# Kernel tuning notes

Measured on AMD Instinct MI355X. Metric: run time of the kernel, lower is better.

Reference implementation:

```python
import jax, jax.numpy as jnp
import numpy as np

B, S, D_MODEL, D_K, D_V, N_HEAD = 2, 2048, 1024, 1024, 1024, 16


def setup_inputs() -> dict:
    key = jax.random.key(0)
    k1, k2, k3, k4, k5, k6, k7 = jax.random.split(key, 7)
    s = 1.0 / np.sqrt(D_MODEL)
    return {
        "q": jax.random.normal(k1, (B, S, D_MODEL), dtype=jnp.float32),
        "k": jax.random.normal(k2, (B, S, D_MODEL), dtype=jnp.float32),
        "v": jax.random.normal(k3, (B, S, D_MODEL), dtype=jnp.float32),
        "Wq": jax.random.normal(k4, (D_MODEL, D_K), dtype=jnp.float32) * s,
        "Wk": jax.random.normal(k5, (D_MODEL, D_K), dtype=jnp.float32) * s,
        "Wv": jax.random.normal(k6, (D_MODEL, D_V), dtype=jnp.float32) * s,
        "Wp": jax.random.normal(k7, (D_V, D_MODEL), dtype=jnp.float32) * (1.0 / np.sqrt(D_V)),
    }


def reference(q, k, v, Wq, Wk, Wv, Wp):
    b, sq, _ = q.shape
    sk = k.shape[1]
    hd_k = D_K // N_HEAD
    hd_v = D_V // N_HEAD
    # Faithful to original: plain row-major reshape (B,S,d) -> (B,H,S,d/H),
    # i.e. the sequence axis is split across heads (as torch .view does here).
    Q = (q @ Wq).reshape(b, N_HEAD, sq, hd_k)
    K = (k @ Wk).reshape(b, N_HEAD, sk, hd_k)
    V = (v @ Wv).reshape(b, N_HEAD, sk, hd_v)
    # No 1/sqrt(d_k) scaling in the original module.
    wei = jnp.einsum('bhqd,bhkd->bhqk', Q, K)
    # causal mask (masked=True): tril(ones(sq, sk))
    causal = jnp.arange(sq)[:, None] >= jnp.arange(sk)[None, :]
    wei = jnp.where(causal[None, None], wei, -jnp.inf)
    att = jnp.einsum('bhqk,bhkd->bhqd', jax.nn.softmax(wei, axis=-1), V)
    out = jnp.swapaxes(att, 1, 2).reshape(b, sq, D_V)
    return out @ Wp
```

## Files before the change

kernel.cpp:

```cpp
#include <hip/hip_runtime.h>
#include <cstdint>
#include <cstddef>


typedef _Float16 f16;
typedef _Float16 f16x8 __attribute__((ext_vector_type(8)));
typedef float f32x4 __attribute__((ext_vector_type(4)));

#define NB 2
#define NS 2048
#define NDM 1024
#define NHEAD 16

__device__ __forceinline__ void gload16(void* lds, const void* g) {
    __builtin_amdgcn_global_load_lds(
        (__attribute__((address_space(1))) void*)g,
        (__attribute__((address_space(3))) void*)lds, 16, 0, 0);
}

__device__ __forceinline__ float fast_exp2(float x) {
#if __has_builtin(__builtin_amdgcn_exp2f)
    return __builtin_amdgcn_exp2f(x);
#else
    return __expf(x * 0.69314718055994531f);
#endif
}

__global__ __launch_bounds__(256) void cast3_kernel(
    const float* __restrict__ s0, const float* __restrict__ s1, const float* __restrict__ s2,
    f16* __restrict__ d0, f16* __restrict__ d1, f16* __restrict__ d2, int nvec)
{
    const float* s = blockIdx.z == 0 ? s0 : (blockIdx.z == 1 ? s1 : s2);
    f16* d        = blockIdx.z == 0 ? d0 : (blockIdx.z == 1 ? d1 : d2);
    int vi = blockIdx.x * 256 + threadIdx.x;
    if (vi >= nvec) return;
    const float4* sp = (const float4*)s;
    float4 a = sp[vi * 2 + 0];
    float4 b = sp[vi * 2 + 1];
    f16x8 h;
    h[0] = (f16)a.x; h[1] = (f16)a.y; h[2] = (f16)a.z; h[3] = (f16)a.w;
    h[4] = (f16)b.x; h[5] = (f16)b.y; h[6] = (f16)b.z; h[7] = (f16)b.w;
    *(f16x8*)(d + (size_t)vi * 8) = h;
}

__global__ __launch_bounds__(256) void tcast4_kernel(
    const float* __restrict__ w0, const float* __restrict__ w1,
    const float* __restrict__ w2, const float* __restrict__ w3,
    f16* __restrict__ t0, f16* __restrict__ t1, f16* __restrict__ t2, f16* __restrict__ t3)
{
    const int n = 1024;
    const float* W; f16* T;
    switch (blockIdx.z) {
        case 0: W = w0; T = t0; break;
        case 1: W = w1; T = t1; break;
        case 2: W = w2; T = t2; break;
        default: W = w3; T = t3; break;
    }
    __shared__ float tile[32][33];
    int tx = threadIdx.x, ty = threadIdx.y;
    int c0 = blockIdx.x * 32, r0 = blockIdx.y * 32;
    #pragma unroll
    for (int i = 0; i < 32; i += 8)
        tile[ty + i][tx] = W[(size_t)(r0 + ty + i) * n + c0 + tx];
    __syncthreads();
    #pragma unroll
    for (int i = 0; i < 32; i += 8)
        T[(size_t)(c0 + ty + i) * n + r0 + tx] = (f16)tile[tx][ty + i];
}

template <typename CT>
__device__ __forceinline__ void gemm_abt_body(
    const f16* __restrict__ A, const f16* __restrict__ Bt, CT* __restrict__ C,
    int M, int N, int K, int bx, int by, float cscale)
{
    __shared__ f16 As[128][64];
    __shared__ f16 Bs[128][64];
    const int tid  = threadIdx.x;
    const int lane = tid & 63, wave = tid >> 6;
    const int quad = lane >> 4, ln = lane & 15;
    const int wm = wave >> 1, wn = wave & 1;
    const int m0 = by * 128, n0 = bx * 128;
    const int r8 = lane >> 3, c8 = lane & 7;
    const int swz = ((c8 ^ r8) * 8);

    f32x4 acc[4][4] = {};
    for (int k0 = 0; k0 < K; k0 += 64) {
        __syncthreads();
        #pragma unroll
        for (int i = 0; i < 4; i++) {
            int blk = wave * 4 + i;
            int row = blk * 8 + r8;
            gload16(&As[blk * 8][0], &A [(size_t)(m0 + row) * K + k0 + swz]);
            gload16(&Bs[blk * 8][0], &Bt[(size_t)(n0 + row) * K + k0 + swz]);
        }
        __syncthreads();
        #pragma unroll
        for (int kc = 0; kc < 2; kc++) {
            f16x8 af[4], bfr[4];
            #pragma unroll
            for (int mt = 0; mt < 4; mt++)
                af[mt] = *(const f16x8*)&As[wm * 64 + mt * 16 + ln][((kc * 4 + quad) ^ (ln & 7)) * 8];
            #pragma unroll
            for (int nt = 0; nt < 4; nt++)
                bfr[nt] = *(const f16x8*)&Bs[wn * 64 + nt * 16 + ln][((kc * 4 + quad) ^ (ln & 7)) * 8];
            #pragma unroll
            for (int mt = 0; mt < 4; mt++)
                #pragma unroll
                for (int nt = 0; nt < 4; nt++)
                    acc[mt][nt] = __builtin_amdgcn_mfma_f32_16x16x32_f16(af[mt], bfr[nt], acc[mt][nt], 0, 0, 0);
        }
    }
    #pragma unroll
    for (int mt = 0; mt < 4; mt++)
        #pragma unroll
        for (int nt = 0; nt < 4; nt++)
            #pragma unroll
            for (int r = 0; r < 4; r++) {
                int row = m0 + wm * 64 + mt * 16 + quad * 4 + r;
                int col = n0 + wn * 64 + nt * 16 + ln;
                C[(size_t)row * N + col] = (CT)(acc[mt][nt][r] * cscale);
            }
}

__global__ __launch_bounds__(256) void gemm3_kernel(
    const f16* __restrict__ a0, const f16* __restrict__ a1, const f16* __restrict__ a2,
    const f16* __restrict__ b0, const f16* __restrict__ b1, const f16* __restrict__ b2,
    f16* __restrict__ c0, f16* __restrict__ c1, f16* __restrict__ c2, int M, int N, int K)
{
    const f16 *A, *Bt; f16* C; float sc;
    switch (blockIdx.z) {
        case 0: A = a0; Bt = b0; C = c0; sc = 1.4426950408889634f; break;
        case 1: A = a1; Bt = b1; C = c1; sc = 1.0f; break;
        default: A = a2; Bt = b2; C = c2; sc = 1.0f; break;
    }
    gemm_abt_body<f16>(A, Bt, C, M, N, K, blockIdx.x, blockIdx.y, sc);
}

__global__ __launch_bounds__(256) void gemm_out_kernel(
    const f16* __restrict__ A, const f16* __restrict__ Bt, float* __restrict__ C, int M, int N, int K)
{
    gemm_abt_body<float>(A, Bt, C, M, N, K, blockIdx.x, blockIdx.y, 1.0f);
}

__global__ __launch_bounds__(256) void vtrans_kernel(
    const f16* __restrict__ Vp, f16* __restrict__ Vt)
{
    const int kt = blockIdx.x;
    const int h  = blockIdx.y;
    const int b  = blockIdx.z;
    const f16* src = Vp + (size_t)b * (NS * NDM) + (size_t)h * (128 * NDM);
    f16* dst = Vt + (size_t)(b * NHEAD + h) * (64 * 2048);

    __shared__ f16 Ls[64][64];
    const int tid = threadIdx.x;
    #pragma unroll
    for (int i = 0; i < 2; i++) {
        int vi = tid + i * 256;
        int key = vi >> 3, c = vi & 7;
        int cs = c ^ ((key >> 3) & 7);
        *(uint4*)&Ls[key][cs * 8] = *(const uint4*)&src[(size_t)(kt * 64 + key) * 64 + c * 8];
    }
    __syncthreads();
    #pragma unroll
    for (int i = 0; i < 2; i++) {
        int vi = tid + i * 256;
        int d2 = vi >> 3, kc = vi & 7;
        int cs = (d2 >> 3) ^ kc;
        f16 tmp[8];
        #pragma unroll
        for (int j = 0; j < 8; j++)
            tmp[j] = Ls[kc * 8 + j][cs * 8 + (d2 & 7)];
        *(uint4*)&dst[(size_t)d2 * 2048 + kt * 64 + kc * 8] = *(uint4*)tmp;
    }
}

__global__ __launch_bounds__(256) void attn_kernel(
    const f16* __restrict__ Qp, const f16* __restrict__ Kp, const f16* __restrict__ Vt,
    f16* __restrict__ att)
{
    const int p = blockIdx.x;
    const int h = blockIdx.y;
    const int b = blockIdx.z;
    const size_t hb = (size_t)b * (NS * NDM) + (size_t)h * (128 * NDM);
    const f16* Qh = Qp + hb;
    const f16* Kh = Kp + hb;
    const f16* Vh = Vt + (size_t)(b * NHEAD + h) * (64 * 2048);

    __shared__ f16 PQ[64][136];
    __shared__ f16 Ks[128][64];
    __shared__ f16 Vs[64][128];

    const int tid  = threadIdx.x;
    const int lane = tid & 63, wave = tid >> 6;
    const int quad = lane >> 4, ln = lane & 15;
    const int r8 = lane >> 3, c8 = lane & 7;
    const int r4 = lane >> 4, c16 = lane & 15;

    for (int pass = 0; pass < 2; pass++) {
        const int qt = pass == 0 ? (31 - p) : p;
        __syncthreads();
        #pragma unroll
        for (int i = 0; i < 2; i++) {
            int vi = tid + i * 256;
            int row = vi >> 3, kk = (vi & 7) * 8;
            *(uint4*)&PQ[row][kk] = *(const uint4*)&Qh[(size_t)(qt * 64 + row) * 64 + kk];
        }
        __syncthreads();
        f16x8 qf[2];
        #pragma unroll
        for (int kc = 0; kc < 2; kc++)
            qf[kc] = *(const f16x8*)&PQ[wave * 16 + ln][kc * 32 + quad * 8];

        float m_i[4], l_i[4];
        #pragma unroll
        for (int r = 0; r < 4; r++) { m_i[r] = -3e30f; l_i[r] = 0.f; }
        f32x4 o[4] = {};

        const int nkt = (qt + 2) >> 1;
        for (int kt = 0; kt < nkt; kt++) {
            __syncthreads();
            #pragma unroll
            for (int i = 0; i < 4; i++) {
                int blk = wave * 4 + i;
                int krow = blk * 8 + r8;
                gload16(&Ks[blk * 8][0], &Kh[(size_t)(kt * 128 + krow) * 64 + ((c8 ^ r8) * 8)]);
                int vrow = blk * 4 + r4;
                gload16(&Vs[blk * 4][0], &Vh[(size_t)vrow * 2048 + kt * 128 + ((c16 ^ (vrow & 15)) * 8)]);
            }
            __syncthreads();

            f32x4 sf[8] = {};
            #pragma unroll
            for (int kc = 0; kc < 2; kc++)
                #pragma unroll
                for (int ct = 0; ct < 8; ct++) {
                    int krow = ct * 16 + ln;
                    f16x8 kf = *(const f16x8*)&Ks[krow][((kc * 4 + quad) ^ (ln & 7)) * 8];
                    sf[ct] = __builtin_amdgcn_mfma_f32_16x16x32_f16(qf[kc], kf, sf[ct], 0, 0, 0);
                }

            if (kt == nkt - 1) {
                #pragma unroll
                for (int ct = 0; ct < 8; ct++) {
                    int jg = kt * 128 + ct * 16 + ln;
                    #pragma unroll
                    for (int r = 0; r < 4; r++) {
                        int ig = qt * 64 + wave * 16 + quad * 4 + r;
                        if (jg > ig) sf[ct][r] = -3e30f;
                    }
                }
            }

            float alpha[4];
            #pragma unroll
            for (int r = 0; r < 4; r++) {
                float tm = sf[0][r];
                #pragma unroll
                for (int ct = 1; ct < 8; ct++) tm = fmaxf(tm, sf[ct][r]);
                #pragma unroll
                for (int off = 1; off < 16; off <<= 1) tm = fmaxf(tm, __shfl_xor(tm, off, 64));
                float mnew = fmaxf(m_i[r], tm);
                float a = fast_exp2(m_i[r] - mnew);
                float rs = 0.f;
                #pragma unroll
                for (int ct = 0; ct < 8; ct++) {
                    float pv = fast_exp2(sf[ct][r] - mnew);
                    sf[ct][r] = pv; rs += pv;
                }
                #pragma unroll
                for (int off = 1; off < 16; off <<= 1) rs += __shfl_xor(rs, off, 64);
                m_i[r] = mnew; l_i[r] = l_i[r] * a + rs; alpha[r] = a;
            }
            #pragma unroll
            for (int vt = 0; vt < 4; vt++)
                #pragma unroll
                for (int r = 0; r < 4; r++) o[vt][r] *= alpha[r];

            #pragma unroll
            for (int ct = 0; ct < 8; ct++)
                #pragma unroll
                for (int r = 0; r < 4; r++)
                    PQ[wave * 16 + quad * 4 + r][ct * 16 + ln] = (f16)sf[ct][r];

            #pragma unroll
            for (int kc = 0; kc < 4; kc++) {
                f16x8 pa = *(const f16x8*)&PQ[wave * 16 + ln][kc * 32 + quad * 8];
                #pragma unroll
                for (int vt = 0; vt < 4; vt++) {
                    int vrow = vt * 16 + ln;
                    f16x8 vb = *(const f16x8*)&Vs[vrow][(((kc * 4 + quad) ^ ln) & 15) * 8];
                    o[vt] = __builtin_amdgcn_mfma_f32_16x16x32_f16(pa, vb, o[vt], 0, 0, 0);
                }
            }
        }

        #pragma unroll
        for (int r = 0; r < 4; r++) {
            float inv = 1.0f / l_i[r];
            int s2 = qt * 64 + wave * 16 + quad * 4 + r;
            #pragma unroll
            for (int vt = 0; vt < 4; vt++) {
                int d2 = vt * 16 + ln;
                att[((size_t)b * NS + s2) * NDM + h * 64 + d2] = (f16)(o[vt][r] * inv);
            }
        }
    }
}

extern "C" void kernel_launch(void* const* d_in, const int* in_sizes, int n_in,
                              void* d_out, int out_size, void* d_ws, size_t ws_size,
                              hipStream_t stream)
{
    const float* q  = (const float*)d_in[0];
    const float* k  = (const float*)d_in[1];
    const float* v  = (const float*)d_in[2];
    const float* Wq = (const float*)d_in[3];
    const float* Wk = (const float*)d_in[4];
    const float* Wv = (const float*)d_in[5];
    const float* Wp = (const float*)d_in[6];
    float* out = (float*)d_out;

    char* ws = (char*)d_ws;
    const size_t MB = 1024 * 1024;
    f16* qb   = (f16*)(ws + 0 * MB);
    f16* kb   = (f16*)(ws + 8 * MB);
    f16* vb   = (f16*)(ws + 16 * MB);
    f16* Wqt  = (f16*)(ws + 24 * MB);
    f16* Wkt  = (f16*)(ws + 26 * MB);
    f16* Wvt  = (f16*)(ws + 28 * MB);
    f16* Wpt  = (f16*)(ws + 30 * MB);
    f16* Qp   = (f16*)(ws + 32 * MB);
    f16* Kp   = (f16*)(ws + 40 * MB);
    f16* Vp   = (f16*)(ws + 48 * MB);
    f16* attb = (f16*)(ws + 56 * MB);
    f16* Vtg  = vb;

    const int M = NB * NS;
    const int N = NDM;
    const int K = NDM;

    cast3_kernel<<<dim3(2048, 1, 3), 256, 0, stream>>>(q, k, v, qb, kb, vb, (M * NDM) / 8);
    tcast4_kernel<<<dim3(32, 32, 4), dim3(32, 8), 0, stream>>>(Wq, Wk, Wv, Wp, Wqt, Wkt, Wvt, Wpt);
    gemm3_kernel<<<dim3(N / 128, M / 128, 3), 256, 0, stream>>>(qb, kb, vb, Wqt, Wkt, Wvt, Qp, Kp, Vp, M, N, K);
    vtrans_kernel<<<dim3(32, NHEAD, NB), 256, 0, stream>>>(Vp, Vtg);
    attn_kernel<<<dim3(16, NHEAD, NB), 256, 0, stream>>>(Qp, Kp, Vtg, attb);
    gemm_out_kernel<<<dim3(N / 128, M / 128, 1), 256, 0, stream>>>(attb, Wpt, out, M, N, K);
}
```

Measured before the change: 235.4 us.

## Split attention KV range into chunks with merge pass; narrow output GEMM tiles

Attention is rewritten from one block handling a paired short and long query tile to one block per query tile and KV chunk of up to 8 key tiles. Partial unnormalized outputs, row maxima and row sums go to workspace, and a new merge kernel combines them. The output projection GEMM gets its own kernel with 128x64 tiles, doubling the grid. Both changes aim to fill more compute units, at the cost of an extra launch, extra partial-result memory traffic, and reuse of workspace regions (qb, Vp).

```diff
diff --git a/kernel.cpp b/kernel.cpp
--- a/kernel.cpp
+++ b/kernel.cpp
@@ -137,9 +137,58 @@
 }
 
 __global__ __launch_bounds__(256) void gemm_out_kernel(
-    const f16* __restrict__ A, const f16* __restrict__ Bt, float* __restrict__ C, int M, int N, int K)
-{
-    gemm_abt_body<float>(A, Bt, C, M, N, K, blockIdx.x, blockIdx.y, 1.0f);
+    const f16* __restrict__ A, const f16* __restrict__ Bt, float* __restrict__ C,
+    int M, int N, int K)
+{
+    __shared__ f16 As[128][64];
+    __shared__ f16 Bs[64][64];
+    const int tid  = threadIdx.x;
+    const int lane = tid & 63, wave = tid >> 6;
+    const int quad = lane >> 4, ln = lane & 15;
+    const int m0 = blockIdx.y * 128, n0 = blockIdx.x * 64;
+    const int r8 = lane >> 3, c8 = lane & 7;
+    const int swz = ((c8 ^ r8) * 8);
+
+    f32x4 acc[2][4] = {};
+    for (int k0 = 0; k0 < K; k0 += 64) {
+        __syncthreads();
+        #pragma unroll
+        for (int i = 0; i < 4; i++) {
+            int blk = wave * 4 + i;
+            gload16(&As[blk * 8][0], &A[(size_t)(m0 + blk * 8 + r8) * K + k0 + swz]);
+        }
+        #pragma unroll
+        for (int i = 0; i < 2; i++) {
+            int blk = wave * 2 + i;
+            gload16(&Bs[blk * 8][0], &Bt[(size_t)(n0 + blk * 8 + r8) * K + k0 + swz]);
+        }
+        __syncthreads();
+        #pragma unroll
+        for (int kc = 0; kc < 2; kc++) {
+            f16x8 af[2], bfr[4];
+            #pragma unroll
+            for (int mt = 0; mt < 2; mt++)
+                af[mt] = *(const f16x8*)&As[wave * 32 + mt * 16 + ln][((kc * 4 + quad) ^ (ln & 7)) * 8];
+            #pragma unroll
+            for (int nt = 0; nt < 4; nt++)
+                bfr[nt] = *(const f16x8*)&Bs[nt * 16 + ln][((kc * 4 + quad) ^ (ln & 7)) * 8];
+            #pragma unroll
+            for (int mt = 0; mt < 2; mt++)
+                #pragma unroll
+                for (int nt = 0; nt < 4; nt++)
+                    acc[mt][nt] = __builtin_amdgcn_mfma_f32_16x16x32_f16(af[mt], bfr[nt], acc[mt][nt], 0, 0, 0);
+        }
+    }
+    #pragma unroll
+    for (int mt = 0; mt < 2; mt++)
+        #pragma unroll
+        for (int nt = 0; nt < 4; nt++)
+            #pragma unroll
+            for (int r = 0; r < 4; r++) {
+                int row = m0 + wave * 32 + mt * 16 + quad * 4 + r;
+                int col = n0 + nt * 16 + ln;
+                C[(size_t)row * N + col] = acc[mt][nt][r];
+            }
 }
 
 __global__ __launch_bounds__(256) void vtrans_kernel(
@@ -176,15 +225,20 @@
 
 __global__ __launch_bounds__(256) void attn_kernel(
     const f16* __restrict__ Qp, const f16* __restrict__ Kp, const f16* __restrict__ Vt,
-    f16* __restrict__ att)
-{
-    const int p = blockIdx.x;
-    const int h = blockIdx.y;
-    const int b = blockIdx.z;
+    f16* __restrict__ Opart, float* __restrict__ Mpart, float* __restrict__ Lpart)
+{
+    const int qt = blockIdx.x;
+    const int chunk = blockIdx.y;
+    const int z = blockIdx.z;
+    const int nkt = (qt + 2) >> 1;
+    const int nch = (nkt + 7) >> 3;
+    if (chunk >= nch) return;
+    const int h = z & 15, b = z >> 4;
+
     const size_t hb = (size_t)b * (NS * NDM) + (size_t)h * (128 * NDM);
     const f16* Qh = Qp + hb;
     const f16* Kh = Kp + hb;
-    const f16* Vh = Vt + (size_t)(b * NHEAD + h) * (64 * 2048);
+    const f16* Vh = Vt + (size_t)z * (64 * 2048);
 
     __shared__ f16 PQ[64][136];
     __shared__ f16 Ks[128][64];
@@ -196,115 +250,163 @@
     const int r8 = lane >> 3, c8 = lane & 7;
     const int r4 = lane >> 4, c16 = lane & 15;
 
-    for (int pass = 0; pass < 2; pass++) {
-        const int qt = pass == 0 ? (31 - p) : p;
-        __syncthreads();
-        #pragma unroll
-        for (int i = 0; i < 2; i++) {
-            int vi = tid + i * 256;
-            int row = vi >> 3, kk = (vi & 7) * 8;
-            *(uint4*)&PQ[row][kk] = *(const uint4*)&Qh[(size_t)(qt * 64 + row) * 64 + kk];
-        }
-        __syncthreads();
-        f16x8 qf[2];
+    #pragma unroll
+    for (int i = 0; i < 2; i++) {
+        int vi = tid + i * 256;
+        int row = vi >> 3, kk = (vi & 7) * 8;
+        *(uint4*)&PQ[row][kk] = *(const uint4*)&Qh[(size_t)(qt * 64 + row) * 64 + kk];
+    }
+    __syncthreads();
+    f16x8 qf[2];
+    #pragma unroll
+    for (int kc = 0; kc < 2; kc++)
+        qf[kc] = *(const f16x8*)&PQ[wave * 16 + ln][kc * 32 + quad * 8];
+
+    float m_i[4], l_i[4];
+    #pragma unroll
+    for (int r = 0; r < 4; r++) { m_i[r] = -3e30f; l_i[r] = 0.f; }
+    f32x4 o[4] = {};
+
+    const int kt0 = chunk * 8;
+    const int kt1 = (kt0 + 8 < nkt) ? (kt0 + 8) : nkt;
+    for (int kt = kt0; kt < kt1; kt++) {
+        __syncthreads();
+        #pragma unroll
+        for (int i = 0; i < 4; i++) {
+            int blk = wave * 4 + i;
+            int krow = blk * 8 + r8;
+            gload16(&Ks[blk * 8][0], &Kh[(size_t)(kt * 128 + krow) * 64 + ((c8 ^ r8) * 8)]);
+            int vrow = blk * 4 + r4;
+            gload16(&Vs[blk * 4][0], &Vh[(size_t)vrow * 2048 + kt * 128 + ((c16 ^ (vrow & 15)) * 8)]);
+        }
+        __syncthreads();
+
+        f32x4 sf[8] = {};
         #pragma unroll
         for (int kc = 0; kc < 2; kc++)
-            qf[kc] = *(const f16x8*)&PQ[wave * 16 + ln][kc * 32 + quad * 8];
-
-        float m_i[4], l_i[4];
-        #pragma unroll
-        for (int r = 0; r < 4; r++) { m_i[r] = -3e30f; l_i[r] = 0.f; }
-        f32x4 o[4] = {};
-
-        const int nkt = (qt + 2) >> 1;
-        for (int kt = 0; kt < nkt; kt++) {
-            __syncthreads();
-            #pragma unroll
-            for (int i = 0; i < 4; i++) {
-                int blk = wave * 4 + i;
-                int krow = blk * 8 + r8;
-                gload16(&Ks[blk * 8][0], &Kh[(size_t)(kt * 128 + krow) * 64 + ((c8 ^ r8) * 8)]);
-                int vrow = blk * 4 + r4;
-                gload16(&Vs[blk * 4][0], &Vh[(size_t)vrow * 2048 + kt * 128 + ((c16 ^ (vrow & 15)) * 8)]);
-            }
-            __syncthreads();
-
-            f32x4 sf[8] = {};
-            #pragma unroll
-            for (int kc = 0; kc < 2; kc++)
+            #pragma unroll
+            for (int ct = 0; ct < 8; ct++) {
+                int krow = ct * 16 + ln;
+                f16x8 kf = *(const f16x8*)&Ks[krow][((kc * 4 + quad) ^ (ln & 7)) * 8];
+                sf[ct] = __builtin_amdgcn_mfma_f32_16x16x32_f16(qf[kc], kf, sf[ct], 0, 0, 0);
+            }
+
+        if (kt == nkt - 1) {
+            #pragma unroll
+            for (int ct = 0; ct < 8; ct++) {
+                int jg = kt * 128 + ct * 16 + ln;
                 #pragma unroll
-                for (int ct = 0; ct < 8; ct++) {
-                    int krow = ct * 16 + ln;
-                    f16x8 kf = *(const f16x8*)&Ks[krow][((kc * 4 + quad) ^ (ln & 7)) * 8];
-                    sf[ct] = __builtin_amdgcn_mfma_f32_16x16x32_f16(qf[kc], kf, sf[ct], 0, 0, 0);
+                for (int r = 0; r < 4; r++) {
+                    int ig = qt * 64 + wave * 16 + quad * 4 + r;
+                    if (jg > ig) sf[ct][r] = -3e30f;
                 }
-
-            if (kt == nkt - 1) {
-                #pragma unroll
-                for (int ct = 0; ct < 8; ct++) {
-                    int jg = kt * 128 + ct * 16 + ln;
-                    #pragma unroll
-                    for (int r = 0; r < 4; r++) {
-                        int ig = qt * 64 + wave * 16 + quad * 4 + r;
-                        if (jg > ig) sf[ct][r] = -3e30f;
-                    }
-                }
-            }
-
-            float alpha[4];
-            #pragma unroll
-            for (int r = 0; r < 4; r++) {
-                float tm = sf[0][r];
-                #pragma unroll
-                for (int ct = 1; ct < 8; ct++) tm = fmaxf(tm, sf[ct][r]);
-                #pragma unroll
-                for (int off = 1; off < 16; off <<= 1) tm = fmaxf(tm, __shfl_xor(tm, off, 64));
-                float mnew = fmaxf(m_i[r], tm);
-                float a = fast_exp2(m_i[r] - mnew);
-                float rs = 0.f;
-                #pragma unroll
-                for (int ct = 0; ct < 8; ct++) {
-                    float pv = fast_exp2(sf[ct][r] - mnew);
-                    sf[ct][r] = pv; rs += pv;
-                }
-                #pragma unroll
-                for (int off = 1; off < 16; off <<= 1) rs += __shfl_xor(rs, off, 64);
-                m_i[r] = mnew; l_i[r] = l_i[r] * a + rs; alpha[r] = a;
-            }
-            #pragma unroll
-            for (int vt = 0; vt < 4; vt++)
-                #pragma unroll
-                for (int r = 0; r < 4; r++) o[vt][r] *= alpha[r];
-
-            #pragma unroll
-            for (int ct = 0; ct < 8; ct++)
-                #pragma unroll
-                for (int r = 0; r < 4; r++)
-                    PQ[wave * 16 + quad * 4 + r][ct * 16 + ln] = (f16)sf[ct][r];
-
-            #pragma unroll
-            for (int kc = 0; kc < 4; kc++) {
-                f16x8 pa = *(const f16x8*)&PQ[wave * 16 + ln][kc * 32 + quad * 8];
-                #pragma unroll
-                for (int vt = 0; vt < 4; vt++) {
-                    int vrow = vt * 16 + ln;
-                    f16x8 vb = *(const f16x8*)&Vs[vrow][(((kc * 4 + quad) ^ ln) & 15) * 8];
-                    o[vt] = __builtin_amdgcn_mfma_f32_16x16x32_f16(pa, vb, o[vt], 0, 0, 0);
-                }
-            }
-        }
-
+            }
+        }
+
+        float alpha[4];
         #pragma unroll
         for (int r = 0; r < 4; r++) {
-            float inv = 1.0f / l_i[r];
-            int s2 = qt * 64 + wave * 16 + quad * 4 + r;
+            float tm = sf[0][r];
+            #pragma unroll
+            for (int ct = 1; ct < 8; ct++) tm = fmaxf(tm, sf[ct][r]);
+            #pragma unroll
+            for (int off = 1; off < 16; off <<= 1) tm = fmaxf(tm, __shfl_xor(tm, off, 64));
+            float mnew = fmaxf(m_i[r], tm);
+            float a = fast_exp2(m_i[r] - mnew);
+            float rs = 0.f;
+            #pragma unroll
+            for (int ct = 0; ct < 8; ct++) {
+                float pv = fast_exp2(sf[ct][r] - mnew);
+                sf[ct][r] = pv; rs += pv;
+            }
+            #pragma unroll
+            for (int off = 1; off < 16; off <<= 1) rs += __shfl_xor(rs, off, 64);
+            m_i[r] = mnew; l_i[r] = l_i[r] * a + rs; alpha[r] = a;
+        }
+        #pragma unroll
+        for (int vt = 0; vt < 4; vt++)
+            #pragma unroll
+            for (int r = 0; r < 4; r++) o[vt][r] *= alpha[r];
+
+        #pragma unroll
+        for (int ct = 0; ct < 8; ct++)
+            #pragma unroll
+            for (int r = 0; r < 4; r++)
+                PQ[wave * 16 + quad * 4 + r][ct * 16 + ln] = (f16)sf[ct][r];
+
+        #pragma unroll
+        for (int kc = 0; kc < 4; kc++) {
+            f16x8 pa = *(const f16x8*)&PQ[wave * 16 + ln][kc * 32 + quad * 8];
             #pragma unroll
             for (int vt = 0; vt < 4; vt++) {
-                int d2 = vt * 16 + ln;
-                att[((size_t)b * NS + s2) * NDM + h * 64 + d2] = (f16)(o[vt][r] * inv);
-            }
-        }
-    }
+                int vrow = vt * 16 + ln;
+                f16x8 vb = *(const f16x8*)&Vs[vrow][(((kc * 4 + quad) ^ ln) & 15) * 8];
+                o[vt] = __builtin_amdgcn_mfma_f32_16x16x32_f16(pa, vb, o[vt], 0, 0, 0);
+            }
+        }
+    }
+
+    const int pid = (z * 32 + qt) * 2 + chunk;
+    f16* Op = Opart + (size_t)pid * 4096;
+    #pragma unroll
+    for (int r = 0; r < 4; r++) {
+        int s2l = wave * 16 + quad * 4 + r;
+        #pragma unroll
+        for (int vt = 0; vt < 4; vt++)
+            Op[s2l * 64 + vt * 16 + ln] = (f16)o[vt][r];
+        if (ln == 0) {
+            Mpart[pid * 64 + s2l] = m_i[r];
+            Lpart[pid * 64 + s2l] = l_i[r];
+        }
+    }
+}
+
+__global__ __launch_bounds__(256) void attn_merge_kernel(
+    const f16* __restrict__ Opart, const float* __restrict__ Mpart, const float* __restrict__ Lpart,
+    f16* __restrict__ att)
+{
+    const int qt = blockIdx.x, z = blockIdx.y;
+    const int h = z & 15, b = z >> 4;
+    const int nkt = (qt + 2) >> 1;
+    const int nch = (nkt + 7) >> 3;
+    const int tid = threadIdx.x;
+    const int r = tid >> 2, cg = (tid & 3) * 16;
+    const int pid0 = (z * 32 + qt) * 2;
+    const f16* O0 = Opart + (size_t)pid0 * 4096 + r * 64 + cg;
+
+    float m0 = Mpart[pid0 * 64 + r], l0 = Lpart[pid0 * 64 + r];
+    float w0 = 1.f, w1 = 0.f, inv;
+    if (nch == 2) {
+        float m1 = Mpart[(pid0 + 1) * 64 + r], l1 = Lpart[(pid0 + 1) * 64 + r];
+        float m = fmaxf(m0, m1);
+        w0 = fast_exp2(m0 - m); w1 = fast_exp2(m1 - m);
+        inv = 1.f / (w0 * l0 + w1 * l1);
+    } else {
+        inv = 1.f / l0;
+    }
+
+    f16x8 a0 = *(const f16x8*)(O0);
+    f16x8 a1 = *(const f16x8*)(O0 + 8);
+    f16x8 outv0, outv1;
+    if (nch == 2) {
+        const f16* O1 = O0 + 4096;
+        f16x8 b0v = *(const f16x8*)(O1);
+        f16x8 b1v = *(const f16x8*)(O1 + 8);
+        #pragma unroll
+        for (int j = 0; j < 8; j++) {
+            outv0[j] = (f16)((w0 * (float)a0[j] + w1 * (float)b0v[j]) * inv);
+            outv1[j] = (f16)((w0 * (float)a1[j] + w1 * (float)b1v[j]) * inv);
+        }
+    } else {
+        #pragma unroll
+        for (int j = 0; j < 8; j++) {
+            outv0[j] = (f16)((float)a0[j] * inv);
+            outv1[j] = (f16)((float)a1[j] * inv);
+        }
+    }
+    f16* dst = att + ((size_t)(b * NS) + qt * 64 + r) * NDM + h * 64 + cg;
+    *(f16x8*)(dst) = outv0;
+    *(f16x8*)(dst + 8) = outv1;
 }
 
 extern "C" void kernel_launch(void* const* d_in, const int* in_sizes, int n_in,
@@ -335,6 +437,10 @@
     f16* attb = (f16*)(ws + 56 * MB);
     f16* Vtg  = vb;
 
+    f16*   Opart = qb;
+    float* Mpart = (float*)(ws + 48 * MB);
+    float* Lpart = (float*)(ws + 49 * MB);
+
     const int M = NB * NS;
     const int N = NDM;
     const int K = NDM;
@@ -343,6 +449,7 @@
     tcast4_kernel<<<dim3(32, 32, 4), dim3(32, 8), 0, stream>>>(Wq, Wk, Wv, Wp, Wqt, Wkt, Wvt, Wpt);
     gemm3_kernel<<<dim3(N / 128, M / 128, 3), 256, 0, stream>>>(qb, kb, vb, Wqt, Wkt, Wvt, Qp, Kp, Vp, M, N, K);
     vtrans_kernel<<<dim3(32, NHEAD, NB), 256, 0, stream>>>(Vp, Vtg);
-    attn_kernel<<<dim3(16, NHEAD, NB), 256, 0, stream>>>(Qp, Kp, Vtg, attb);
-    gemm_out_kernel<<<dim3(N / 128, M / 128, 1), 256, 0, stream>>>(attb, Wpt, out, M, N, K);
-}
+    attn_kernel<<<dim3(32, 2, 32), 256, 0, stream>>>(Qp, Kp, Vtg, Opart, Mpart, Lpart);
+    attn_merge_kernel<<<dim3(32, 32), 256, 0, stream>>>(Opart, Mpart, Lpart, attb);
+    gemm_out_kernel<<<dim3(N / 64, M / 128), 256, 0, stream>>>(attb, Wpt, out, M, N, K);
+}
```

Measured after the change: 271.7 us. 1.15x slower.
